# Performance work log

Hardware: AMD Instinct MI355X
Metric: run time of the kernel (lower is better)

The kernel has to match this reference:

```python
import jax, jax.numpy as jnp
import numpy as np

B, N, C, T = 512, 62, 8, 64
K = 8          # topk
HEADS = 4
OUT = 128
EPS = 1e-5     # BatchNorm1d eps
NEG_SLOPE = 0.2  # GATConv leaky_relu slope


def _gat(x, W, a_src, a_dst, bias, src, dst, valid, num_nodes, concat):
    """PyG GATConv (eval mode, self-loops already in edge list)."""
    H, Co = a_src.shape[1], a_src.shape[2]
    xl = (x @ W.T).reshape(num_nodes, H, Co)          # [V,H,Co]
    al_src = jnp.sum(xl * a_src, axis=-1)             # [V,H]
    al_dst = jnp.sum(xl * a_dst, axis=-1)             # [V,H]
    alpha = jax.nn.leaky_relu(al_src[src] + al_dst[dst], NEG_SLOPE)  # [E,H]
    alpha = jnp.where(valid[:, None], alpha, -jnp.inf)
    amax = jax.ops.segment_max(alpha, dst, num_segments=num_nodes)   # [V,H]
    ex = jnp.where(valid[:, None], jnp.exp(alpha - amax[dst]), 0.0)
    denom = jax.ops.segment_sum(ex, dst, num_segments=num_nodes)     # [V,H]
    w = ex / denom[dst]                                              # softmax per dst
    out = jax.ops.segment_sum(xl[src] * w[:, :, None], dst, num_segments=num_nodes)
    out = out.reshape(num_nodes, H * Co) if concat else out.mean(axis=1)
    return out + bias


def reference(x, edge_index, W1, W2, b_sp, V_sp, bn_w, bn_b,
              g1_w, g1_asrc, g1_adst, g1_b, g2_w, g2_asrc, g2_adst, g2_b):
    # edge_index is unused: spatial=True rebuilds the graph from attention.
    x4 = x.reshape(B, N, C, T)
    # SpatialAttention: ((x @ W1) @ W2) -> tanh(. @ V + b) -> BatchNorm1d(N)
    prod = jnp.einsum('bnct,t->bnc', x4, W1) @ W2      # [B,N,N]
    S = jnp.tanh(prod @ V_sp + b_sp)                   # [B,N,N]
    mean = S.mean(axis=(0, 2), keepdims=True)          # BN over channel dim 1
    var = S.var(axis=(0, 2), keepdims=True)
    adj = (S - mean) / jnp.sqrt(var + EPS) * bn_w[None, :, None] + bn_b[None, :, None]
    # topk mask + dense_to_sparse: exactly K edges per (batch, row)
    _, idx = jax.lax.top_k(adj, K)                     # [B,N,K] column indices
    offs = (jnp.arange(B) * N)[:, None, None]
    src = (jnp.broadcast_to(jnp.arange(N)[None, :, None], (B, N, K)) + offs).reshape(-1)
    dst = (idx + offs).reshape(-1)
    # GATConv: remove_self_loops then add_self_loops -> mask topk self-edges, append loops
    loops = jnp.arange(B * N)
    valid = jnp.concatenate([src != dst, jnp.ones(B * N, dtype=bool)])
    src = jnp.concatenate([src, loops])
    dst = jnp.concatenate([dst, loops])
    h = x4.reshape(B * N, C * T)
    h = jax.nn.relu(_gat(h, g1_w, g1_asrc, g1_adst, g1_b, src, dst, valid, B * N, True))
    h = jax.nn.relu(_gat(h, g2_w, g2_asrc, g2_adst, g2_b, src, dst, valid, B * N, False))
    return h


def setup_inputs() -> dict:
    key = jax.random.key(0)
    ks = jax.random.split(key, 16)
    d_in = C * T  # 512
    return {
        'x': jax.random.normal(ks[0], (B, N, C, T), jnp.float32),
        'edge_index': jax.random.randint(ks[1], (2, 128), 0, B * N, jnp.int64) if False else jax.random.randint(ks[1], (2, 128), 0, B * N).astype(jnp.int32),
        'W1': jax.random.uniform(ks[2], (T,), jnp.float32),
        'W2': jax.random.normal(ks[3], (C, N), jnp.float32) * 0.1,
        'b_sp': jax.random.normal(ks[4], (1, N, N), jnp.float32) * 0.1,
        'V_sp': jax.random.normal(ks[5], (N, N), jnp.float32) * 0.1,
        'bn_w': jnp.ones((N,), jnp.float32),
        'bn_b': jnp.zeros((N,), jnp.float32),
        'g1_w': jax.random.normal(ks[6], (HEADS * OUT, d_in), jnp.float32) * 0.04,
        'g1_asrc': jax.random.normal(ks[7], (1, HEADS, OUT), jnp.float32) * 0.06,
        'g1_adst': jax.random.normal(ks[8], (1, HEADS, OUT), jnp.float32) * 0.06,
        'g1_b': jnp.zeros((HEADS * OUT,), jnp.float32),
        'g2_w': jax.random.normal(ks[9], (HEADS * OUT, HEADS * OUT), jnp.float32) * 0.04,
        'g2_asrc': jax.random.normal(ks[10], (1, HEADS, OUT), jnp.float32) * 0.06,
        'g2_adst': jax.random.normal(ks[11], (1, HEADS, OUT), jnp.float32) * 0.06,
        'g2_b': jnp.zeros((OUT,), jnp.float32),
    }
```

## Files before the change

### kernel.cpp

```cpp
#include <hip/hip_runtime.h>
#include <math.h>

#define B_ 512
#define N_ 62
#define V_ (B_ * N_)
#define TOPK_ 8

typedef __attribute__((ext_vector_type(8))) short bf16x8;
typedef __attribute__((ext_vector_type(4))) float f32x4;

__device__ __forceinline__ unsigned short bf16rn(float f) {
    unsigned int u = __float_as_uint(f);
    unsigned int r = (u + 0x7fffu + ((u >> 16) & 1u)) >> 16;
    return (unsigned short)r;
}
__device__ __forceinline__ float bf16tof(unsigned short h) {
    return __uint_as_float(((unsigned int)h) << 16);
}

__device__ __forceinline__ void gload16(const void* g, void* l) {
    __builtin_amdgcn_global_load_lds(
        (const __attribute__((address_space(1))) unsigned int*)g,
        (__attribute__((address_space(3))) unsigned int*)l, 16, 0, 0);
}

__global__ __launch_bounds__(256) void spatial_S(
    const float* __restrict__ x, const float* __restrict__ W1,
    const float* __restrict__ W2, const float* __restrict__ bsp,
    const float* __restrict__ Vsp, float* __restrict__ S,
    unsigned short* __restrict__ A2)
{
    int w = threadIdx.x >> 6, lane = threadIdx.x & 63;
    int blk = blockIdx.x * 4 + w;
    int n = blk % N_;
    const float* xr = x + (size_t)blk * 512;
    float w1 = W1[lane];

    float y[8];
#pragma unroll
    for (int c = 0; c < 8; ++c) {
        float xv = xr[c * 64 + lane];
        A2[(size_t)blk * 512 + c * 64 + lane] = bf16rn(xv);
        float p = xv * w1;
#pragma unroll
        for (int off = 32; off; off >>= 1) p += __shfl_xor(p, off);
        y[c] = p;
    }

    __shared__ float pr[4][N_];
    if (lane < N_) {
        float acc = 0.f;
#pragma unroll
        for (int c = 0; c < 8; ++c) acc += y[c] * W2[c * N_ + lane];
        pr[w][lane] = acc;
    }
    __syncthreads();
    if (lane < N_) {
        float acc = bsp[n * N_ + lane];
        for (int k = 0; k < N_; ++k) acc += pr[w][k] * Vsp[k * N_ + lane];
        S[(size_t)blk * N_ + lane] = tanhf(acc);
    }
}

__global__ __launch_bounds__(256) void bn_part(
    const float* __restrict__ S, double* __restrict__ part)
{
    int n = blockIdx.x >> 4, slice = blockIdx.x & 15;
    double s = 0.0, s2 = 0.0;
    int i0 = slice * 1984;
    for (int i = i0 + threadIdx.x; i < i0 + 1984; i += 256) {
        int b = i / N_, m = i - b * N_;
        float v = S[((size_t)b * N_ + n) * N_ + m];
        s += v; s2 += (double)v * v;
    }
    __shared__ double sh[256], sh2[256];
    sh[threadIdx.x] = s; sh2[threadIdx.x] = s2;
    __syncthreads();
    for (int off = 128; off; off >>= 1) {
        if (threadIdx.x < off) {
            sh[threadIdx.x] += sh[threadIdx.x + off];
            sh2[threadIdx.x] += sh2[threadIdx.x + off];
        }
        __syncthreads();
    }
    if (threadIdx.x == 0) {
        part[((size_t)n * 16 + slice) * 2 + 0] = sh[0];
        part[((size_t)n * 16 + slice) * 2 + 1] = sh2[0];
    }
}

__global__ __launch_bounds__(64) void bn_final(
    const double* __restrict__ part, const float* __restrict__ bnw,
    const float* __restrict__ bnb, float* __restrict__ scale,
    float* __restrict__ shift)
{
    int n = threadIdx.x;
    if (n >= N_) return;
    double s = 0.0, s2 = 0.0;
    for (int j = 0; j < 16; ++j) {
        s  += part[((size_t)n * 16 + j) * 2 + 0];
        s2 += part[((size_t)n * 16 + j) * 2 + 1];
    }
    const double cnt = (double)(B_ * N_);
    double mean = s / cnt;
    double var = s2 / cnt - mean * mean;
    float inv = (float)(1.0 / sqrt(var + 1e-5));
    scale[n] = bnw[n] * inv;
    shift[n] = bnb[n] - (float)mean * bnw[n] * inv;
}

__global__ __launch_bounds__(64) void topk_mask(
    const float* __restrict__ S, const float* __restrict__ scale,
    const float* __restrict__ shift, unsigned long long* __restrict__ maskT)
{
    int blk = blockIdx.x;
    int b = blk / N_, n = blk - b * N_;
    int lane = threadIdx.x;
    float v = (lane < N_) ? S[(size_t)blk * N_ + lane] * scale[n] + shift[n]
                          : -INFINITY;
    bool sel = false;
#pragma unroll
    for (int k = 0; k < TOPK_; ++k) {
        float mv = v; int mi = lane;
#pragma unroll
        for (int off = 32; off; off >>= 1) {
            float ov = __shfl_xor(mv, off);
            int   oi = __shfl_xor(mi, off);
            if (ov > mv || (ov == mv && oi < mi)) { mv = ov; mi = oi; }
        }
        if (lane == mi) { sel = true; v = -INFINITY; }
    }
    unsigned long long row = __ballot(sel) | (1ull << n);
    if (lane < N_ && ((row >> lane) & 1ull))
        atomicOr(&maskT[(size_t)b * N_ + lane], 1ull << n);
}

__global__ __launch_bounds__(256) void zero_u64(unsigned long long* p, int n)
{
    int i = blockIdx.x * 256 + threadIdx.x;
    if (i < n) p[i] = 0ull;
}

__global__ __launch_bounds__(256) void split_pair(
    const float* __restrict__ in, unsigned short* __restrict__ out, int total4)
{
    int gid = blockIdx.x * 256 + threadIdx.x;
    if (gid >= total4) return;
    int row = gid >> 7;
    int c = (gid & 127) * 4;
    float4 v = ((const float4*)in)[gid];
    ushort4 h, l;
    float f;
    h.x = bf16rn(v.x); f = v.x - bf16tof(h.x); l.x = bf16rn(f);
    h.y = bf16rn(v.y); f = v.y - bf16tof(h.y); l.y = bf16rn(f);
    h.z = bf16rn(v.z); f = v.z - bf16tof(h.z); l.z = bf16rn(f);
    h.w = bf16rn(v.w); f = v.w - bf16tof(h.w); l.w = bf16rn(f);
    *(ushort4*)(&out[(size_t)row * 1024 + c])       = h;
    *(ushort4*)(&out[(size_t)row * 1024 + 512 + c]) = l;
}

__global__ __launch_bounds__(256) void gemm_bf16(
    const unsigned short* __restrict__ Ah, const unsigned short* __restrict__ Bw,
    unsigned short* __restrict__ Cs)
{
    __shared__ __align__(16) unsigned short smem[16384];
    char* As = (char*)smem;
    char* Bs = (char*)(smem + 8192);

    int tid = threadIdx.x;
    int lane = tid & 63, w = tid >> 6;

    int flat = blockIdx.y * 4 + blockIdx.x;
    int swz = (flat & 7) * 124 + (flat >> 3);
    int by = swz >> 2, bx = swz & 3;
    int bm = by * 128, bn = bx * 128;

    int wr = w >> 1, wc = w & 1;

    f32x4 acc[4][4];
#pragma unroll
    for (int mf = 0; mf < 4; ++mf)
#pragma unroll
        for (int nf = 0; nf < 4; ++nf) acc[mf][nf] = (f32x4){0.f, 0.f, 0.f, 0.f};

    int srow = w * 8 + (lane >> 3);
    int kcol = (lane & 7) ^ (lane >> 3);
    int ldsoff = w * 1024;

    for (int kt = 0; kt < 16; ++kt) {
        int k0 = (kt & 7) * 64;
        int bBase = (kt >> 3) * 512 + k0;
#pragma unroll
        for (int i = 0; i < 4; ++i) {
            int row = i * 32 + srow;
            gload16(Ah + (size_t)(bm + row) * 512 + k0 + kcol * 8,
                    As + i * 4096 + ldsoff);
            gload16(Bw + (size_t)(bn + row) * 1024 + bBase + kcol * 8,
                    Bs + i * 4096 + ldsoff);
        }
        __syncthreads();

#pragma unroll
        for (int kk = 0; kk < 2; ++kk) {
            bf16x8 af[4], bfr[4];
#pragma unroll
            for (int mf = 0; mf < 4; ++mf)
                af[mf] = *(const bf16x8*)(As + (wr*64 + mf*16 + (lane&15))*128
                                             + ((kk*4 + (lane>>4)) ^ (lane&7))*16);
#pragma unroll
            for (int nf = 0; nf < 4; ++nf)
                bfr[nf] = *(const bf16x8*)(Bs + (wc*64 + nf*16 + (lane&15))*128
                                              + ((kk*4 + (lane>>4)) ^ (lane&7))*16);
#pragma unroll
            for (int mf = 0; mf < 4; ++mf)
#pragma unroll
                for (int nf = 0; nf < 4; ++nf)
                    acc[mf][nf] = __builtin_amdgcn_mfma_f32_16x16x32_bf16(
                        af[mf], bfr[nf], acc[mf][nf], 0, 0, 0);
        }
        __syncthreads();
    }

    int r0 = bm + wr * 64 + (lane >> 4) * 4;
    int c0 = bn + wc * 64 + (lane & 15);
#pragma unroll
    for (int mf = 0; mf < 4; ++mf)
#pragma unroll
        for (int nf = 0; nf < 4; ++nf)
#pragma unroll
            for (int r = 0; r < 4; ++r) {
                float v = acc[mf][nf][r];
                unsigned short h = bf16rn(v);
                unsigned short l = bf16rn(v - bf16tof(h));
                size_t row = (size_t)(r0 + mf * 16 + r);
                Cs[row * 1024 + c0 + nf * 16] = h;
                Cs[row * 1024 + 512 + c0 + nf * 16] = l;
            }
}

template <int APPLY>
__global__ __launch_bounds__(512, 8) void gat_aggM(
    const unsigned short* __restrict__ XL,
    const float* __restrict__ asrc, const float* __restrict__ adst,
    const unsigned long long* __restrict__ maskT,
    const float* __restrict__ bias,
    void* __restrict__ outp)
{
    __shared__ __align__(16) char lds[34816];
    float* av  = (float*)(lds);
    float* dv  = (float*)(lds + 2080);
    float* shs = (float*)(lds + 32768);
    float* shd = (float*)(lds + 33792);

    int b = blockIdx.x;
    int tid = threadIdx.x;
    int lane = tid & 63, w = tid >> 6;
    const unsigned short* base = XL + (size_t)b * N_ * 1024;

    av[w * 65 + lane] = asrc[tid];
    dv[w * 65 + lane] = adst[tid];
    __syncthreads();

    {
        int s = tid >> 3, sl = tid & 7;
        const unsigned short* xp = base + (size_t)s * 1024 + sl * 64;
        float ps = 0.f, pd = 0.f;
        union V8 { uint4 u; unsigned short s[8]; };
#pragma unroll
        for (int g = 0; g < 8; ++g) {
            V8 vh, vl;
            vh.u = *(const uint4*)(xp + g * 8);
            vl.u = *(const uint4*)(xp + 512 + g * 8);
            const float* avp = av + sl * 65 + g * 8;
            const float* dvp = dv + sl * 65 + g * 8;
#pragma unroll
            for (int j = 0; j < 8; ++j) {
                float xv = bf16tof(vh.s[j]) + bf16tof(vl.s[j]);
                ps += xv * avp[j];
                pd += xv * dvp[j];
            }
        }
        ps += __shfl_xor(ps, 1);
        pd += __shfl_xor(pd, 1);
        if ((sl & 1) == 0) {
            shs[s * 4 + (sl >> 1)] = ps;
            shd[s * 4 + (sl >> 1)] = pd;
        }
    }
    __syncthreads();

    for (int t = w; t < 248; t += 8) {
        int d = t >> 2, h = t & 3;
        unsigned long long m = maskT[(size_t)b * N_ + d];
        bool valid = (lane < N_) && ((m >> lane) & 1ull);
        float a = -INFINITY;
        if (valid) {
            float raw = shs[lane * 4 + h] + shd[d * 4 + h];
            a = (raw > 0.f) ? raw : 0.2f * raw;
        }
        float mx = a;
#pragma unroll
        for (int off = 32; off; off >>= 1) mx = fmaxf(mx, __shfl_xor(mx, off));
        float ex = valid ? expf(a - mx) : 0.f;
        float sm = ex;
#pragma unroll
        for (int off = 32; off; off >>= 1) sm += __shfl_xor(sm, off);
        float wv = valid ? ex / sm : 0.f;
        int addr = h * 8192 + d * 128
                 + (((lane >> 3) ^ (d & 7)) << 4) + ((lane & 7) << 1);
        *(unsigned short*)(lds + addr) = bf16rn(wv);
    }
    __syncthreads();

    int cc = lane & 15, lh = lane >> 4;

    union U8 { unsigned short s[8]; bf16x8 v; };

    f32x4 acc[4];
#pragma unroll
    for (int mf = 0; mf < 4; ++mf) acc[mf] = (f32x4){0.f, 0.f, 0.f, 0.f};

#pragma unroll
    for (int ch = 0; ch < 4; ++ch) {
        if (APPLY == 1 && ch > 0) {
#pragma unroll
            for (int mf = 0; mf < 4; ++mf) acc[mf] = (f32x4){0.f, 0.f, 0.f, 0.f};
        }

        const unsigned short* xp = base + (size_t)(lh * 8) * 1024
                                        + ch * 128 + w * 16 + cc;
#pragma unroll
        for (int kk = 0; kk < 2; ++kk) {
            U8 bh, bl;
#pragma unroll
            for (int j = 0; j < 8; ++j) {
                size_t o = (size_t)(kk * 32 + j) * 1024;
                bh.s[j] = xp[o];
                bl.s[j] = xp[o + 512];
            }
            bf16x8 af[4];
#pragma unroll
            for (int mf = 0; mf < 4; ++mf)
                af[mf] = *(const bf16x8*)(lds + ch * 8192
                              + (mf * 16 + cc) * 128
                              + (((kk * 4 + lh) ^ (cc & 7)) << 4));
#pragma unroll
            for (int mf = 0; mf < 4; ++mf) {
                acc[mf] = __builtin_amdgcn_mfma_f32_16x16x32_bf16(
                    af[mf], bh.v, acc[mf], 0, 0, 0);
                acc[mf] = __builtin_amdgcn_mfma_f32_16x16x32_bf16(
                    af[mf], bl.v, acc[mf], 0, 0, 0);
            }
        }

        if (APPLY == 1) {
            int c = ch * 128 + w * 16 + cc;
            float bc = bias[c];
            unsigned short* H = (unsigned short*)outp;
#pragma unroll
            for (int mf = 0; mf < 4; ++mf)
#pragma unroll
                for (int r = 0; r < 4; ++r) {
                    int d = mf * 16 + lh * 4 + r;
                    if (d < N_) {
                        float v = acc[mf][r] + bc;
                        v = v > 0.f ? v : 0.f;
                        H[(size_t)(b * N_ + d) * 512 + c] = bf16rn(v);
                    }
                }
        }
    }

    if (APPLY == 0) {
        int c = w * 16 + cc;
        float bc = bias[c];
        float* outF = (float*)outp;
#pragma unroll
        for (int mf = 0; mf < 4; ++mf)
#pragma unroll
            for (int r = 0; r < 4; ++r) {
                int d = mf * 16 + lh * 4 + r;
                if (d < N_) {
                    float v = acc[mf][r] * 0.25f + bc;
                    outF[(size_t)(b * N_ + d) * 128 + c] = v > 0.f ? v : 0.f;
                }
            }
    }
}

extern "C" void kernel_launch(void* const* d_in, const int* in_sizes, int n_in,
                              void* d_out, int out_size, void* d_ws, size_t ws_size,
                              hipStream_t stream)
{
    const float* x    = (const float*)d_in[0];
    const float* W1   = (const float*)d_in[2];
    const float* W2   = (const float*)d_in[3];
    const float* bsp  = (const float*)d_in[4];
    const float* Vsp  = (const float*)d_in[5];
    const float* bnw  = (const float*)d_in[6];
    const float* bnb  = (const float*)d_in[7];
    const float* g1w  = (const float*)d_in[8];
    const float* g1as = (const float*)d_in[9];
    const float* g1ad = (const float*)d_in[10];
    const float* g1b  = (const float*)d_in[11];
    const float* g2w  = (const float*)d_in[12];
    const float* g2as = (const float*)d_in[13];
    const float* g2ad = (const float*)d_in[14];
    const float* g2b  = (const float*)d_in[15];
    float* out = (float*)d_out;

    char* ws = (char*)d_ws;
    size_t off = 0;
    auto alloc = [&](size_t bytes) -> void* {
        void* p = ws + off;
        off += (bytes + 255) & ~(size_t)255;
        return p;
    };
    float* S      = (float*)alloc((size_t)V_ * N_ * 4);
    float* scale  = (float*)alloc(N_ * 4);
    float* shift  = (float*)alloc(N_ * 4);
    double* part  = (double*)alloc((size_t)N_ * 16 * 2 * 8);
    unsigned long long* maskT = (unsigned long long*)alloc((size_t)V_ * 8);
    unsigned short* A2  = (unsigned short*)alloc((size_t)V_ * 512 * 2);
    unsigned short* Bw1 = (unsigned short*)alloc((size_t)512 * 1024 * 2);
    unsigned short* Bw2 = (unsigned short*)alloc((size_t)512 * 1024 * 2);
    unsigned short* XL  = (unsigned short*)alloc((size_t)(V_ + 2) * 1024 * 2);
    unsigned short* H1  = (unsigned short*)alloc((size_t)V_ * 512 * 2);

    zero_u64<<<(V_ + 255) / 256, 256, 0, stream>>>(maskT, V_);
    spatial_S<<<V_ / 4, 256, 0, stream>>>(x, W1, W2, bsp, Vsp, S, A2);
    bn_part<<<N_ * 16, 256, 0, stream>>>(S, part);
    bn_final<<<1, 64, 0, stream>>>(part, bnw, bnb, scale, shift);
    topk_mask<<<V_, 64, 0, stream>>>(S, scale, shift, maskT);

    split_pair<<<(512 * 128 + 255) / 256, 256, 0, stream>>>(g1w, Bw1, 512 * 128);
    split_pair<<<(512 * 128 + 255) / 256, 256, 0, stream>>>(g2w, Bw2, 512 * 128);

    dim3 gg(4, 248);
    gemm_bf16<<<gg, 256, 0, stream>>>(A2, Bw1, XL);
    gat_aggM<1><<<B_, 512, 0, stream>>>(XL, g1as, g1ad, maskT, g1b, H1);

    gemm_bf16<<<gg, 256, 0, stream>>>(H1, Bw2, XL);
    gat_aggM<0><<<B_, 512, 0, stream>>>(XL, g2as, g2ad, maskT, g2b, out);
}
```

Baseline: 412.3 us.

## Pad nodes per graph, transpose GEMM output, fuse attention logits into epilogue

Each graph's 62 nodes are padded to 64 rows, so every GEMM tile of 128 rows covers exactly two graphs. The GEMM epilogue now writes its output transposed per graph (channel-major, node contiguous) and computes the per-head source and destination attention dot products, accumulating them with atomics. The aggregation kernel then reads precomputed logits instead of re-reading the full feature rows, and loads B fragments as 16-byte vectors instead of strided scalar gathers. The cost is extra zeroing launches, float atomics, and about 3% padded GEMM work. The padding rows in A2 and H1 are never written, so whatever they hold flows into the padded rows' logits, though those rows are never read.

```diff
diff --git a/kernel.cpp b/kernel.cpp
--- a/kernel.cpp
+++ b/kernel.cpp
@@ -4,6 +4,7 @@
 #define B_ 512
 #define N_ 62
 #define V_ (B_ * N_)
+#define MP_ (B_ * 64)
 #define TOPK_ 8
 
 typedef __attribute__((ext_vector_type(8))) short bf16x8;
@@ -32,7 +33,7 @@
 {
     int w = threadIdx.x >> 6, lane = threadIdx.x & 63;
     int blk = blockIdx.x * 4 + w;
-    int n = blk % N_;
+    int b = blk / N_, n = blk - b * N_;
     const float* xr = x + (size_t)blk * 512;
     float w1 = W1[lane];
 
@@ -40,7 +41,7 @@
 #pragma unroll
     for (int c = 0; c < 8; ++c) {
         float xv = xr[c * 64 + lane];
-        A2[(size_t)blk * 512 + c * 64 + lane] = bf16rn(xv);
+        A2[((size_t)(b * 64 + n)) * 512 + c * 64 + lane] = bf16rn(xv);
         float p = xv * w1;
 #pragma unroll
         for (int off = 32; off; off >>= 1) p += __shfl_xor(p, off);
@@ -161,7 +162,9 @@
 
 __global__ __launch_bounds__(256) void gemm_bf16(
     const unsigned short* __restrict__ Ah, const unsigned short* __restrict__ Bw,
-    unsigned short* __restrict__ Cs)
+    unsigned short* __restrict__ XT,
+    const float* __restrict__ asrc, const float* __restrict__ adst,
+    float* __restrict__ als, float* __restrict__ ald)
 {
     __shared__ __align__(16) unsigned short smem[16384];
     char* As = (char*)smem;
@@ -171,7 +174,7 @@
     int lane = tid & 63, w = tid >> 6;
 
     int flat = blockIdx.y * 4 + blockIdx.x;
-    int swz = (flat & 7) * 124 + (flat >> 3);
+    int swz = (flat & 7) * 128 + (flat >> 3);
     int by = swz >> 2, bx = swz & 3;
     int bm = by * 128, bn = bx * 128;
 
@@ -221,71 +224,75 @@
         __syncthreads();
     }
 
-    int r0 = bm + wr * 64 + (lane >> 4) * 4;
-    int c0 = bn + wc * 64 + (lane & 15);
-#pragma unroll
-    for (int mf = 0; mf < 4; ++mf)
-#pragma unroll
-        for (int nf = 0; nf < 4; ++nf)
+    int cc = lane & 15, lh = lane >> 4;
+    int bb = (bm >> 6) + wr;
+    int c0 = bn + wc * 64 + cc;
+    int hH = bn >> 7;
+    float as4[4], ad4[4];
+#pragma unroll
+    for (int nf = 0; nf < 4; ++nf) {
+        as4[nf] = asrc[c0 + nf * 16];
+        ad4[nf] = adst[c0 + nf * 16];
+    }
+
+#pragma unroll
+    for (int mf = 0; mf < 4; ++mf) {
+        int s = lh * 4 + mf * 16;
+        f32x4 ts = (f32x4){0.f, 0.f, 0.f, 0.f};
+        f32x4 td = (f32x4){0.f, 0.f, 0.f, 0.f};
+#pragma unroll
+        for (int nf = 0; nf < 4; ++nf) {
+            ushort4 hv, lv;
 #pragma unroll
             for (int r = 0; r < 4; ++r) {
                 float v = acc[mf][nf][r];
-                unsigned short h = bf16rn(v);
-                unsigned short l = bf16rn(v - bf16tof(h));
-                size_t row = (size_t)(r0 + mf * 16 + r);
-                Cs[row * 1024 + c0 + nf * 16] = h;
-                Cs[row * 1024 + 512 + c0 + nf * 16] = l;
+                unsigned short hb = bf16rn(v);
+                ((unsigned short*)&hv)[r] = hb;
+                ((unsigned short*)&lv)[r] = bf16rn(v - bf16tof(hb));
+                ts[r] += v * as4[nf];
+                td[r] += v * ad4[nf];
             }
+            size_t cb = ((size_t)bb * 1024 + c0 + nf * 16) * 64 + s;
+            *(ushort4*)(XT + cb) = hv;
+            *(ushort4*)(XT + cb + (size_t)512 * 64) = lv;
+        }
+#pragma unroll
+        for (int off = 1; off < 16; off <<= 1) {
+#pragma unroll
+            for (int r = 0; r < 4; ++r) {
+                ts[r] += __shfl_xor(ts[r], off);
+                td[r] += __shfl_xor(td[r], off);
+            }
+        }
+        if (cc == 0) {
+#pragma unroll
+            for (int r = 0; r < 4; ++r) {
+                atomicAdd(&als[((size_t)bb * 64 + s + r) * 4 + hH], ts[r]);
+                atomicAdd(&ald[((size_t)bb * 64 + s + r) * 4 + hH], td[r]);
+            }
+        }
+    }
 }
 
 template <int APPLY>
 __global__ __launch_bounds__(512, 8) void gat_aggM(
-    const unsigned short* __restrict__ XL,
-    const float* __restrict__ asrc, const float* __restrict__ adst,
+    const unsigned short* __restrict__ XT,
+    const float* __restrict__ als, const float* __restrict__ ald,
     const unsigned long long* __restrict__ maskT,
     const float* __restrict__ bias,
     void* __restrict__ outp)
 {
     __shared__ __align__(16) char lds[34816];
-    float* av  = (float*)(lds);
-    float* dv  = (float*)(lds + 2080);
     float* shs = (float*)(lds + 32768);
     float* shd = (float*)(lds + 33792);
 
     int b = blockIdx.x;
     int tid = threadIdx.x;
     int lane = tid & 63, w = tid >> 6;
-    const unsigned short* base = XL + (size_t)b * N_ * 1024;
-
-    av[w * 65 + lane] = asrc[tid];
-    dv[w * 65 + lane] = adst[tid];
-    __syncthreads();
-
-    {
-        int s = tid >> 3, sl = tid & 7;
-        const unsigned short* xp = base + (size_t)s * 1024 + sl * 64;
-        float ps = 0.f, pd = 0.f;
-        union V8 { uint4 u; unsigned short s[8]; };
-#pragma unroll
-        for (int g = 0; g < 8; ++g) {
-            V8 vh, vl;
-            vh.u = *(const uint4*)(xp + g * 8);
-            vl.u = *(const uint4*)(xp + 512 + g * 8);
-            const float* avp = av + sl * 65 + g * 8;
-            const float* dvp = dv + sl * 65 + g * 8;
-#pragma unroll
-            for (int j = 0; j < 8; ++j) {
-                float xv = bf16tof(vh.s[j]) + bf16tof(vl.s[j]);
-                ps += xv * avp[j];
-                pd += xv * dvp[j];
-            }
-        }
-        ps += __shfl_xor(ps, 1);
-        pd += __shfl_xor(pd, 1);
-        if ((sl & 1) == 0) {
-            shs[s * 4 + (sl >> 1)] = ps;
-            shd[s * 4 + (sl >> 1)] = pd;
-        }
+
+    if (tid < 256) {
+        shs[tid] = als[(size_t)b * 256 + tid];
+        shd[tid] = ald[(size_t)b * 256 + tid];
     }
     __syncthreads();
 
@@ -313,8 +320,9 @@
     __syncthreads();
 
     int cc = lane & 15, lh = lane >> 4;
-
-    union U8 { unsigned short s[8]; bf16x8 v; };
+    const unsigned short* xb = XT + (size_t)b * 1024 * 64;
+
+    union U16 { uint4 u; bf16x8 v; };
 
     f32x4 acc[4];
 #pragma unroll
@@ -327,17 +335,13 @@
             for (int mf = 0; mf < 4; ++mf) acc[mf] = (f32x4){0.f, 0.f, 0.f, 0.f};
         }
 
-        const unsigned short* xp = base + (size_t)(lh * 8) * 1024
-                                        + ch * 128 + w * 16 + cc;
+        const unsigned short* xp = xb + ((size_t)(ch * 128 + w * 16 + cc)) * 64
+                                      + lh * 8;
 #pragma unroll
         for (int kk = 0; kk < 2; ++kk) {
-            U8 bh, bl;
-#pragma unroll
-            for (int j = 0; j < 8; ++j) {
-                size_t o = (size_t)(kk * 32 + j) * 1024;
-                bh.s[j] = xp[o];
-                bl.s[j] = xp[o + 512];
-            }
+            U16 bh, bl;
+            bh.u = *(const uint4*)(xp + kk * 32);
+            bl.u = *(const uint4*)(xp + kk * 32 + (size_t)512 * 64);
             bf16x8 af[4];
 #pragma unroll
             for (int mf = 0; mf < 4; ++mf)
@@ -365,7 +369,7 @@
                     if (d < N_) {
                         float v = acc[mf][r] + bc;
                         v = v > 0.f ? v : 0.f;
-                        H[(size_t)(b * N_ + d) * 512 + c] = bf16rn(v);
+                        H[((size_t)b * 64 + d) * 512 + c] = bf16rn(v);
                     }
                 }
         }
@@ -382,7 +386,7 @@
                 int d = mf * 16 + lh * 4 + r;
                 if (d < N_) {
                     float v = acc[mf][r] * 0.25f + bc;
-                    outF[(size_t)(b * N_ + d) * 128 + c] = v > 0.f ? v : 0.f;
+                    outF[((size_t)b * N_ + d) * 128 + c] = v > 0.f ? v : 0.f;
                 }
             }
     }
@@ -421,13 +425,18 @@
     float* shift  = (float*)alloc(N_ * 4);
     double* part  = (double*)alloc((size_t)N_ * 16 * 2 * 8);
     unsigned long long* maskT = (unsigned long long*)alloc((size_t)V_ * 8);
-    unsigned short* A2  = (unsigned short*)alloc((size_t)V_ * 512 * 2);
+    float* als    = (float*)alloc((size_t)MP_ * 4 * 4);
+    float* ald    = (float*)alloc((size_t)MP_ * 4 * 4);
+    unsigned short* A2  = (unsigned short*)alloc((size_t)MP_ * 512 * 2);
     unsigned short* Bw1 = (unsigned short*)alloc((size_t)512 * 1024 * 2);
     unsigned short* Bw2 = (unsigned short*)alloc((size_t)512 * 1024 * 2);
-    unsigned short* XL  = (unsigned short*)alloc((size_t)(V_ + 2) * 1024 * 2);
-    unsigned short* H1  = (unsigned short*)alloc((size_t)V_ * 512 * 2);
+    unsigned short* XT  = (unsigned short*)alloc((size_t)B_ * 1024 * 64 * 2 + 256);
+    unsigned short* H1  = (unsigned short*)alloc((size_t)MP_ * 512 * 2);
 
     zero_u64<<<(V_ + 255) / 256, 256, 0, stream>>>(maskT, V_);
+    zero_u64<<<(MP_ * 4 * 2 / 2 + 255) / 256, 256, 0, stream>>>(
+        (unsigned long long*)als, MP_ * 4 * 2 / 2);
+
     spatial_S<<<V_ / 4, 256, 0, stream>>>(x, W1, W2, bsp, Vsp, S, A2);
     bn_part<<<N_ * 16, 256, 0, stream>>>(S, part);
     bn_final<<<1, 64, 0, stream>>>(part, bnw, bnb, scale, shift);
@@ -436,10 +445,12 @@
     split_pair<<<(512 * 128 + 255) / 256, 256, 0, stream>>>(g1w, Bw1, 512 * 128);
     split_pair<<<(512 * 128 + 255) / 256, 256, 0, stream>>>(g2w, Bw2, 512 * 128);
 
-    dim3 gg(4, 248);
-    gemm_bf16<<<gg, 256, 0, stream>>>(A2, Bw1, XL);
-    gat_aggM<1><<<B_, 512, 0, stream>>>(XL, g1as, g1ad, maskT, g1b, H1);
-
-    gemm_bf16<<<gg, 256, 0, stream>>>(H1, Bw2, XL);
-    gat_aggM<0><<<B_, 512, 0, stream>>>(XL, g2as, g2ad, maskT, g2b, out);
-}
+    dim3 gg(4, 256);
+    gemm_bf16<<<gg, 256, 0, stream>>>(A2, Bw1, XT, g1as, g1ad, als, ald);
+    gat_aggM<1><<<B_, 512, 0, stream>>>(XT, als, ald, maskT, g1b, H1);
+
+    zero_u64<<<(MP_ * 4 * 2 / 2 + 255) / 256, 256, 0, stream>>>(
+        (unsigned long long*)als, MP_ * 4 * 2 / 2);
+    gemm_bf16<<<gg, 256, 0, stream>>>(H1, Bw2, XT, g2as, g2ad, als, ald);
+    gat_aggM<0><<<B_, 512, 0, stream>>>(XT, als, ald, maskT, g2b, out);
+}
```

Result: slower. 446.9 us (+8.4%).
